# Kernel optimization log

Measured on AMD Instinct MI355X. Metric: run time of the kernel, lower is better.

## Reference

```python
import jax, jax.numpy as jnp
import numpy as np

DIM = 384
HEADS = 8
B, H, W = 2, 128, 128


def _conv(x, w, groups=1):
    # x: [B,C,H,W], w: [Cout, Cin//groups, kh, kw]
    return jax.lax.conv_general_dilated(
        x, w, window_strides=(1, 1), padding='SAME',
        feature_group_count=groups,
        dimension_numbers=('NCHW', 'OIHW', 'NCHW'))


def setup_inputs() -> dict:
    key = jax.random.key(0)
    ks = jax.random.split(key, 12)
    C = DIM
    s = 0.05
    inp = {
        'prompt_feat': jax.random.normal(ks[0], (B, C, H, W), jnp.float32),
        'x_mod': jax.random.normal(ks[1], (B, C, H, W), jnp.float32),
        'y': jax.random.normal(ks[2], (B, C, H, W), jnp.float32),
        'q1_w': jax.random.normal(ks[3], (C, C, 1, 1), jnp.float32) * s,
        'q2_w': jax.random.normal(ks[4], (C, C, 1, 1), jnp.float32) * s,
        'q_dw_w': jax.random.normal(ks[5], (C, 1, 3, 3), jnp.float32) * s,
        'gate_dw_w': jax.random.normal(ks[6], (2 * C, 1, 3, 3), jnp.float32) * s,
        'gate_pw_w': jax.random.normal(ks[7], (C, 2 * C, 1, 1), jnp.float32) * s,
        'kv_w': jax.random.normal(ks[8], (2 * C, C, 1, 1), jnp.float32) * s,
        'kv_dw_w': jax.random.normal(ks[9], (2 * C, 1, 3, 3), jnp.float32) * s,
        'proj_w': jax.random.normal(ks[10], (C, C, 1, 1), jnp.float32) * s,
        'temperature': jnp.ones((HEADS, 1, 1), jnp.float32),
    }
    return inp


def _l2norm(x, eps=1e-12):
    n = jnp.sqrt(jnp.sum(x * x, axis=-1, keepdims=True))
    return x / jnp.maximum(n, eps)


def reference(prompt_feat, x_mod, y, q1_w, q2_w, q_dw_w, gate_dw_w, gate_pw_w,
              kv_w, kv_dw_w, proj_w, temperature):
    b, c, h, w = x_mod.shape
    head = HEADS
    q1 = _conv(prompt_feat, q1_w)              # [B,C,H,W]
    q2 = _conv(x_mod, q2_w)                    # [B,C,H,W]
    cat = jnp.concatenate([q1, q2], axis=1)    # [B,2C,H,W]
    gate = jax.nn.sigmoid(_conv(_conv(cat, gate_dw_w, groups=2 * c), gate_pw_w))
    q = _conv(gate * q1 + (1.0 - gate) * q2, q_dw_w, groups=c)
    kv = _conv(_conv(y, kv_w), kv_dw_w, groups=2 * c)
    k, v = jnp.split(kv, 2, axis=1)            # each [B,C,H,W]
    # rearrange to [B, head, C//head, H*W]
    def to_heads(t):
        return t.reshape(b, head, c // head, h * w)
    q = _l2norm(to_heads(q))
    k = _l2norm(to_heads(k))
    v = to_heads(v)
    # channel attention: [B, head, d, d] with d = C//head
    attn = jnp.einsum('bhcn,bhdn->bhcd', q, k) * temperature[None]
    attn = jax.nn.softmax(attn, axis=-1)
    out = jnp.einsum('bhcd,bhdn->bhcn', attn, v)
    out = out.reshape(b, c, h, w)
    return _conv(out, proj_w)
```

## Files before the change

### kernel.cpp

```cpp
#include <hip/hip_runtime.h>
#include <math.h>

#define HW   16384
#define IMW  128
#define IMH  128
#define CC   384
#define CC2  768
#define NH   8
#define DH   48

typedef unsigned short u16;
typedef __attribute__((ext_vector_type(8))) short short8;
typedef __attribute__((ext_vector_type(16))) float f32x16;

__device__ __forceinline__ void gld16(const u16* g, u16* l) {
    __builtin_amdgcn_global_load_lds(
        (const __attribute__((address_space(1))) unsigned int*)(uintptr_t)g,
        (__attribute__((address_space(3))) unsigned int*)(uintptr_t)l, 16, 0, 0);
}

__device__ __forceinline__ void bf16split(float x, unsigned& hb16, unsigned& lb16) {
    const unsigned u = __float_as_uint(x);
    const unsigned hb = (u + 0x7FFFu + ((u >> 16) & 1u)) & 0xFFFF0000u;
    const float lo = x - __uint_as_float(hb);
    const unsigned v = __float_as_uint(lo);
    hb16 = hb >> 16;
    lb16 = ((v + 0x7FFFu + ((v >> 16) & 1u)) >> 16) & 0xFFFFu;
}

__global__ void wsplit_k(const float* __restrict__ w0, const float* __restrict__ w1,
                         const float* __restrict__ w2, const float* __restrict__ w3,
                         const float* __restrict__ w4,
                         u16* __restrict__ Wh, u16* __restrict__ Wl)
{
    const int i = blockIdx.x * 256 + threadIdx.x;
    if (i >= 1032192) return;
    float x;
    if (i < 147456)      x = w0[i];
    else if (i < 294912) x = w1[i - 147456];
    else if (i < 589824) x = w2[i - 294912];
    else if (i < 884736) x = w3[i - 589824];
    else                 x = w4[i - 884736];
    unsigned h, l;
    bf16split(x, h, l);
    Wh[i] = (u16)h;
    Wl[i] = (u16)l;
}

__global__ __launch_bounds__(256)
void trsplit_k(const float* __restrict__ X, u16* __restrict__ XTh,
               u16* __restrict__ XTl, int C)
{
    __shared__ float tl[64][65];
    const int t  = threadIdx.x;
    const int n0 = blockIdx.x * 64;
    const int k0 = blockIdx.y * 64;
    #pragma unroll
    for (int p = 0; p < 4; ++p) {
        const int kk = p * 16 + (t >> 4);
        const int nn = (t & 15) * 4;
        *(float4*)&tl[kk][nn] = *(const float4*)(X + (size_t)(k0 + kk) * HW + n0 + nn);
    }
    __syncthreads();
    const int n    = t >> 2;
    const int kseg = (t & 3) * 16;
    const int gn   = n0 + n;
    #pragma unroll
    for (int h = 0; h < 2; ++h) {
        unsigned hw_[4], lw_[4];
        #pragma unroll
        for (int i2 = 0; i2 < 4; ++i2) {
            unsigned hp = 0, lp = 0;
            #pragma unroll
            for (int e = 0; e < 2; ++e) {
                unsigned hb, lb;
                bf16split(tl[kseg + h * 8 + i2 * 2 + e][n], hb, lb);
                hp |= hb << (16 * e);
                lp |= lb << (16 * e);
            }
            hw_[i2] = hp; lw_[i2] = lp;
        }
        const int kb = k0 + kseg + h * 8;
        const size_t off = (size_t)gn * C + kb;
        *(uint4*)(XTh + off) = make_uint4(hw_[0], hw_[1], hw_[2], hw_[3]);
        *(uint4*)(XTl + off) = make_uint4(lw_[0], lw_[1], lw_[2], lw_[3]);
    }
}

template<int GATE>
__global__ __launch_bounds__(256, 2)
void gemm_mfma_k(const u16* __restrict__ Wh, const u16* __restrict__ Wl,
                 const u16* __restrict__ XTh, const u16* __restrict__ XTl,
                 int K, float* __restrict__ Out,
                 const float* __restrict__ q1p, const float* __restrict__ q2p)
{
    __shared__ u16 Ah[2][4096], Al[2][4096], Bh[2][4096], Bl[2][4096];
    const int t = threadIdx.x;
    const int w = t >> 6;
    const int l = t & 63;
    const int l31 = l & 31, lh = l >> 5;
    const int nBase = blockIdx.x * 128;
    const int mBase = blockIdx.y * 128;
    const int wmh = (w >> 1) * 2;
    const int wnh = (w & 1) * 2;

    const int jj0 = w * 2, jj1 = jj0 + 1;
    const int offA0 = (mBase + (jj0 & 3) * 32 + l31) * K + (jj0 >> 2) * 16 + lh * 8;
    const int offA1 = (mBase + (jj1 & 3) * 32 + l31) * K + (jj1 >> 2) * 16 + lh * 8;
    const int offB0 = (nBase + (jj0 & 3) * 32 + l31) * K + (jj0 >> 2) * 16 + lh * 8;
    const int offB1 = (nBase + (jj1 & 3) * 32 + l31) * K + (jj1 >> 2) * 16 + lh * 8;
    const int ldst0 = jj0 * 512, ldst1 = jj1 * 512;

#define STAGE(buf, k0)                                  \
    do {                                                \
        gld16(Wh  + offA0 + (k0), Ah[buf] + ldst0);     \
        gld16(Wh  + offA1 + (k0), Ah[buf] + ldst1);     \
        gld16(Wl  + offA0 + (k0), Al[buf] + ldst0);     \
        gld16(Wl  + offA1 + (k0), Al[buf] + ldst1);     \
        gld16(XTh + offB0 + (k0), Bh[buf] + ldst0);     \
        gld16(XTh + offB1 + (k0), Bh[buf] + ldst1);     \
        gld16(XTl + offB0 + (k0), Bl[buf] + ldst0);     \
        gld16(XTl + offB1 + (k0), Bl[buf] + ldst1);     \
    } while (0)

    f32x16 acc[2][2];
    #pragma unroll
    for (int i = 0; i < 2; ++i)
        #pragma unroll
        for (int j = 0; j < 2; ++j)
            #pragma unroll
            for (int r = 0; r < 16; ++r) acc[i][j][r] = 0.f;

    const int NC = K >> 5;
    STAGE(0, 0);
    __syncthreads();
    int p = 0;
    for (int c = 0; c < NC; ++c) {
        if (c + 1 < NC) STAGE(p ^ 1, (c + 1) * 32);

        short8 ah[2][2], al[2][2], bh[2][2], bl[2][2];
        #pragma unroll
        for (int ks = 0; ks < 2; ++ks)
            #pragma unroll
            for (int fm = 0; fm < 2; ++fm) {
                const int ia = (ks * 4 + wmh + fm) * 512 + l * 8;
                ah[fm][ks] = *(const short8*)(&Ah[p][ia]);
                al[fm][ks] = *(const short8*)(&Al[p][ia]);
            }
        #pragma unroll
        for (int ks = 0; ks < 2; ++ks)
            #pragma unroll
            for (int fn = 0; fn < 2; ++fn) {
                const int ib = (ks * 4 + wnh + fn) * 512 + l * 8;
                bh[fn][ks] = *(const short8*)(&Bh[p][ib]);
                bl[fn][ks] = *(const short8*)(&Bl[p][ib]);
            }
        #pragma unroll
        for (int ks = 0; ks < 2; ++ks)
            #pragma unroll
            for (int fm = 0; fm < 2; ++fm)
                #pragma unroll
                for (int fn = 0; fn < 2; ++fn) {
                    acc[fm][fn] = __builtin_amdgcn_mfma_f32_32x32x16_bf16(ah[fm][ks], bh[fn][ks], acc[fm][fn], 0, 0, 0);
                    acc[fm][fn] = __builtin_amdgcn_mfma_f32_32x32x16_bf16(ah[fm][ks], bl[fn][ks], acc[fm][fn], 0, 0, 0);
                    acc[fm][fn] = __builtin_amdgcn_mfma_f32_32x32x16_bf16(al[fm][ks], bh[fn][ks], acc[fm][fn], 0, 0, 0);
                }
        __syncthreads();
        p ^= 1;
    }
#undef STAGE

    #pragma unroll
    for (int fm = 0; fm < 2; ++fm)
        #pragma unroll
        for (int fn = 0; fn < 2; ++fn) {
            const int mb = mBase + (wmh + fm) * 32 + lh * 4;
            const int nb = nBase + (wnh + fn) * 32 + l31;
            #pragma unroll
            for (int r = 0; r < 16; ++r) {
                const int m = mb + (r & 3) + 8 * (r >> 2);
                float v = acc[fm][fn][r];
                const size_t off = (size_t)m * HW + nb;
                if (GATE) {
                    const float g = 1.f / (1.f + expf(-v));
                    v = g * q1p[off] + (1.f - g) * q2p[off];
                }
                Out[off] = v;
            }
        }
}

__global__ __launch_bounds__(256)
void dw3x3_k(const float* __restrict__ in, const float* __restrict__ w9,
             float* __restrict__ out)
{
    const int c  = blockIdx.y;
    const int y0 = blockIdx.x * 8;
    __shared__ float tile[10][IMW];

    const float* inc = in + (size_t)c * HW;
    for (int i = threadIdx.x; i < 10 * IMW; i += 256) {
        const int ry = i >> 7, rx = i & 127;
        const int gy = y0 + ry - 1;
        tile[ry][rx] = ((unsigned)gy < (unsigned)IMH) ? inc[gy * IMW + rx] : 0.f;
    }
    float w[9];
    #pragma unroll
    for (int i = 0; i < 9; ++i) w[i] = w9[c * 9 + i];
    __syncthreads();

    const int x  = threadIdx.x & 127;
    const int r0 = threadIdx.x >> 7;
    #pragma unroll
    for (int kk = 0; kk < 4; ++kk) {
        const int ry = r0 * 4 + kk;
        float s = 0.f;
        #pragma unroll
        for (int dy = 0; dy < 3; ++dy) {
            #pragma unroll
            for (int dx = 0; dx < 3; ++dx) {
                const int xx = x + dx - 1;
                const float v = ((unsigned)xx < (unsigned)IMW) ? tile[ry + dy][xx] : 0.f;
                s += w[dy * 3 + dx] * v;
            }
        }
        out[(size_t)c * HW + (y0 + ry) * IMW + x] = s;
    }
}

__global__ __launch_bounds__(256)
void gram_k(const float* __restrict__ q, const float* __restrict__ k,
            float* __restrict__ S, float* __restrict__ ssq, float* __restrict__ ssk)
{
    const int h = blockIdx.y;
    __shared__ float qs[48][65];
    __shared__ float ks[48][65];
    const int t   = threadIdx.x;
    const int tdd = t & 15;
    const int tcc = t >> 4;

    float acc[3][3];
    #pragma unroll
    for (int i = 0; i < 3; ++i)
        #pragma unroll
        for (int j = 0; j < 3; ++j) acc[i][j] = 0.f;
    float sq = 0.f, sk = 0.f;

    for (int ch = 0; ch < 8; ++ch) {
        const int n0 = (blockIdx.x + ch * 32) * 64;
        __syncthreads();
        for (int i = t; i < 48 * 16; i += 256) {
            const int cc = i >> 4, f4 = (i & 15) * 4;
            const float4 qv = *(const float4*)(q + (size_t)(h * 48 + cc) * HW + n0 + f4);
            const float4 kv = *(const float4*)(k + (size_t)(h * 48 + cc) * HW + n0 + f4);
            qs[cc][f4 + 0] = qv.x; qs[cc][f4 + 1] = qv.y; qs[cc][f4 + 2] = qv.z; qs[cc][f4 + 3] = qv.w;
            ks[cc][f4 + 0] = kv.x; ks[cc][f4 + 1] = kv.y; ks[cc][f4 + 2] = kv.z; ks[cc][f4 + 3] = kv.w;
        }
        __syncthreads();
        #pragma unroll 4
        for (int n = 0; n < 64; ++n) {
            float qv[3], kv[3];
            #pragma unroll
            for (int j = 0; j < 3; ++j) { qv[j] = qs[tcc + 16 * j][n]; kv[j] = ks[tdd + 16 * j][n]; }
            #pragma unroll
            for (int i = 0; i < 3; ++i)
                #pragma unroll
                for (int j = 0; j < 3; ++j)
                    acc[i][j] += qv[i] * kv[j];
        }
        if (t < 48) {
            float s = 0.f;
            #pragma unroll 8
            for (int n = 0; n < 64; ++n) s += qs[t][n] * qs[t][n];
            sq += s;
        } else if (t >= 128 && t < 176) {
            const int cc = t - 128;
            float s = 0.f;
            #pragma unroll 8
            for (int n = 0; n < 64; ++n) s += ks[cc][n] * ks[cc][n];
            sk += s;
        }
    }
    #pragma unroll
    for (int i = 0; i < 3; ++i)
        #pragma unroll
        for (int j = 0; j < 3; ++j)
            atomicAdd(&S[(size_t)(h * 48 + tcc + 16 * i) * 48 + tdd + 16 * j], acc[i][j]);
    if (t < 48)                   atomicAdd(&ssq[h * 48 + t], sq);
    else if (t >= 128 && t < 176) atomicAdd(&ssk[h * 48 + t - 128], sk);
}

__global__ void softmax_k(float* __restrict__ S, const float* __restrict__ ssq,
                          const float* __restrict__ ssk, const float* __restrict__ temp)
{
    const int h  = blockIdx.x;
    const int cc = threadIdx.x;
    if (cc >= 48) return;
    const float rq = 1.f / fmaxf(sqrtf(ssq[h * 48 + cc]), 1e-12f);
    const float T  = temp[h];
    float l[48];
    float mx = -1e30f;
    #pragma unroll
    for (int d = 0; d < 48; ++d) {
        const float rk = 1.f / fmaxf(sqrtf(ssk[h * 48 + d]), 1e-12f);
        const float v  = S[(size_t)(h * 48 + cc) * 48 + d] * rq * rk * T;
        l[d] = v;
        mx = fmaxf(mx, v);
    }
    float sum = 0.f;
    #pragma unroll
    for (int d = 0; d < 48; ++d) { const float e = expf(l[d] - mx); l[d] = e; sum += e; }
    const float inv = 1.f / sum;
    #pragma unroll
    for (int d = 0; d < 48; ++d) S[(size_t)(h * 48 + cc) * 48 + d] = l[d] * inv;
}

__global__ __launch_bounds__(256)
void attnv_k(const float* __restrict__ A, const float* __restrict__ v,
             float* __restrict__ out)
{
    const int h  = blockIdx.y;
    const int n0 = blockIdx.x * 64;
    __shared__ float As[48][48];
    __shared__ float Vs[48][64];
    const int t = threadIdx.x;

    for (int i = t; i < 48 * 12; i += 256) {
        const int cc = i / 12, d4 = (i % 12) * 4;
        *(float4*)&As[cc][d4] = *(const float4*)(A + (size_t)(h * 48 + cc) * 48 + d4);
    }
    for (int i = t; i < 48 * 16; i += 256) {
        const int dd = i >> 4, f4 = (i & 15) * 4;
        *(float4*)&Vs[dd][f4] = *(const float4*)(v + (size_t)(h * 48 + dd) * HW + n0 + f4);
    }
    __syncthreads();

    const int n4 = (t & 15) * 4;
    const int cg = t >> 4;
    float o[3][4];
    #pragma unroll
    for (int i = 0; i < 3; ++i)
        #pragma unroll
        for (int j = 0; j < 4; ++j) o[i][j] = 0.f;

    #pragma unroll
    for (int d0 = 0; d0 < 48; d0 += 8) {
        float vr[8][4];
        #pragma unroll
        for (int di = 0; di < 8; ++di) {
            const float4 x = *(const float4*)&Vs[d0 + di][n4];
            vr[di][0] = x.x; vr[di][1] = x.y; vr[di][2] = x.z; vr[di][3] = x.w;
        }
        #pragma unroll
        for (int ci = 0; ci < 3; ++ci) {
            const int cc = cg * 3 + ci;
            const float4 a0 = *(const float4*)&As[cc][d0];
            const float4 a1 = *(const float4*)&As[cc][d0 + 4];
            const float a[8] = {a0.x, a0.y, a0.z, a0.w, a1.x, a1.y, a1.z, a1.w};
            #pragma unroll
            for (int di = 0; di < 8; ++di)
                #pragma unroll
                for (int j = 0; j < 4; ++j)
                    o[ci][j] += a[di] * vr[di][j];
        }
    }
    #pragma unroll
    for (int ci = 0; ci < 3; ++ci) {
        const int cc = cg * 3 + ci;
        *(float4*)(out + (size_t)(h * 48 + cc) * HW + n0 + n4) =
            make_float4(o[ci][0], o[ci][1], o[ci][2], o[ci][3]);
    }
}

extern "C" void kernel_launch(void* const* d_in, const int* in_sizes, int n_in,
                              void* d_out, int out_size, void* d_ws, size_t ws_size,
                              hipStream_t stream)
{
    const float* prompt    = (const float*)d_in[0];
    const float* xmod      = (const float*)d_in[1];
    const float* yin       = (const float*)d_in[2];
    const float* q1_w      = (const float*)d_in[3];
    const float* q2_w      = (const float*)d_in[4];
    const float* q_dw_w    = (const float*)d_in[5];
    const float* gate_dw_w = (const float*)d_in[6];
    const float* gate_pw_w = (const float*)d_in[7];
    const float* kv_w      = (const float*)d_in[8];
    const float* kv_dw_w   = (const float*)d_in[9];
    const float* proj_w    = (const float*)d_in[10];
    const float* temp      = (const float*)d_in[11];
    float* out = (float*)d_out;
    float* ws  = (float*)d_ws;

    const size_t BUF  = (size_t)CC2 * HW;
    const size_t HALF = (size_t)CC * HW;
    float* q12 = ws;
    float* t1  = ws + BUF;
    float* t2  = ws + 2 * BUF;
    u16*   Wh  = (u16*)(ws + 3 * BUF);
    u16*   Wl  = Wh + 1032192;
    float* S   = ws + 3 * BUF + 1032192;
    float* ssq = S + NH * DH * DH;
    float* ssk = ssq + CC;

    const int WO_Q1 = 0, WO_Q2 = 147456, WO_GATE = 294912, WO_KV = 589824, WO_PROJ = 884736;

    u16* XT2h = (u16*)t2;
    u16* XT2l = XT2h + (size_t)HW * CC2;
    u16* XT1h = (u16*)t1;
    u16* XT1l = XT1h + (size_t)HW * CC;

    const dim3 blk(256);

    wsplit_k<<<dim3(4032), blk, 0, stream>>>(q1_w, q2_w, gate_pw_w, kv_w, proj_w, Wh, Wl);

    for (int b = 0; b < 2; ++b) {
        const size_t ib = (size_t)b * CC * HW;

        trsplit_k<<<dim3(256, 6), blk, 0, stream>>>(prompt + ib, XT1h, XT1l, CC);
        gemm_mfma_k<0><<<dim3(128, 3), blk, 0, stream>>>(Wh + WO_Q1, Wl + WO_Q1, XT1h, XT1l, CC, q12, nullptr, nullptr);
        trsplit_k<<<dim3(256, 6), blk, 0, stream>>>(xmod + ib, XT1h, XT1l, CC);
        gemm_mfma_k<0><<<dim3(128, 3), blk, 0, stream>>>(Wh + WO_Q2, Wl + WO_Q2, XT1h, XT1l, CC, q12 + HALF, nullptr, nullptr);
        dw3x3_k<<<dim3(16, CC2), blk, 0, stream>>>(q12, gate_dw_w, t1);
        trsplit_k<<<dim3(256, 12), blk, 0, stream>>>(t1, XT2h, XT2l, CC2);
        gemm_mfma_k<1><<<dim3(128, 3), blk, 0, stream>>>(Wh + WO_GATE, Wl + WO_GATE, XT2h, XT2l, CC2, q12, q12, q12 + HALF);
        dw3x3_k<<<dim3(16, CC), blk, 0, stream>>>(q12, q_dw_w, q12 + HALF);
        trsplit_k<<<dim3(256, 6), blk, 0, stream>>>(yin + ib, XT1h, XT1l, CC);
        gemm_mfma_k<0><<<dim3(128, 6), blk, 0, stream>>>(Wh + WO_KV, Wl + WO_KV, XT1h, XT1l, CC, t2, nullptr, nullptr);
        dw3x3_k<<<dim3(16, CC2), blk, 0, stream>>>(t2, kv_dw_w, t1);
        hipMemsetAsync(S, 0, (NH * DH * DH + 2 * CC) * sizeof(float), stream);
        gram_k<<<dim3(32, NH), blk, 0, stream>>>(q12 + HALF, t1, S, ssq, ssk);
        softmax_k<<<dim3(NH), dim3(64), 0, stream>>>(S, ssq, ssk, temp);
        attnv_k<<<dim3(HW / 64, NH), blk, 0, stream>>>(S, t1 + HALF, t2);
        trsplit_k<<<dim3(256, 6), blk, 0, stream>>>(t2, XT1h, XT1l, CC);
        gemm_mfma_k<0><<<dim3(128, 3), blk, 0, stream>>>(Wh + WO_PROJ, Wl + WO_PROJ, XT1h, XT1l, CC, out + ib, nullptr, nullptr);
    }
}
```

Baseline: 889.9 us.

## Pre-tile GEMM operands into LDS-order blocks and swizzle workgroup mapping

```diff
diff --git a/kernel.cpp b/kernel.cpp
--- a/kernel.cpp
+++ b/kernel.cpp
@@ -28,23 +28,39 @@
     lb16 = ((v + 0x7FFFu + ((v >> 16) & 1u)) >> 16) & 0xFFFFu;
 }
 
+
 __global__ void wsplit_k(const float* __restrict__ w0, const float* __restrict__ w1,
                          const float* __restrict__ w2, const float* __restrict__ w3,
                          const float* __restrict__ w4,
                          u16* __restrict__ Wh, u16* __restrict__ Wl)
 {
     const int i = blockIdx.x * 256 + threadIdx.x;
-    if (i >= 1032192) return;
-    float x;
-    if (i < 147456)      x = w0[i];
-    else if (i < 294912) x = w1[i - 147456];
-    else if (i < 589824) x = w2[i - 294912];
-    else if (i < 884736) x = w3[i - 589824];
-    else                 x = w4[i - 884736];
-    unsigned h, l;
-    bf16split(x, h, l);
-    Wh[i] = (u16)h;
-    Wl[i] = (u16)l;
+    if (i >= 129024) return;
+    const float* src; int j, K, wo;
+    if (i < 18432)       { src = w0; j = i;          K = 384; wo = 0; }
+    else if (i < 36864)  { src = w1; j = i - 18432;  K = 384; wo = 147456; }
+    else if (i < 73728)  { src = w2; j = i - 36864;  K = 768; wo = 294912; }
+    else if (i < 110592) { src = w3; j = i - 73728;  K = 384; wo = 589824; }
+    else                 { src = w4; j = i - 110592; K = 384; wo = 884736; }
+    const int kpo = K >> 3;
+    const int m  = j / kpo;
+    const int k  = (j % kpo) * 8;
+
+    unsigned hp[4], lp[4];
+    #pragma unroll
+    for (int q = 0; q < 4; ++q) {
+        unsigned h0, l0, h1, l1;
+        bf16split(src[(size_t)m * K + k + q * 2],     h0, l0);
+        bf16split(src[(size_t)m * K + k + q * 2 + 1], h1, l1);
+        hp[q] = h0 | (h1 << 16);
+        lp[q] = l0 | (l1 << 16);
+    }
+    const int NC = K >> 5, mtile = m >> 7, ml = m & 127;
+    const int c = k >> 5, ks = (k >> 4) & 1, oct = (k >> 3) & 1;
+    const int jj = ks * 4 + (ml >> 5), lo = ml & 31;
+    const size_t off = (size_t)wo + ((size_t)(mtile * NC + c)) * 4096 + jj * 512 + oct * 256 + lo * 8;
+    *(uint4*)(Wh + off) = make_uint4(hp[0], hp[1], hp[2], hp[3]);
+    *(uint4*)(Wl + off) = make_uint4(lp[0], lp[1], lp[2], lp[3]);
 }
 
 __global__ __launch_bounds__(256)
@@ -55,6 +71,7 @@
     const int t  = threadIdx.x;
     const int n0 = blockIdx.x * 64;
     const int k0 = blockIdx.y * 64;
+    const int NC = C >> 5;
     #pragma unroll
     for (int p = 0; p < 4; ++p) {
         const int kk = p * 16 + (t >> 4);
@@ -64,24 +81,28 @@
     __syncthreads();
     const int n    = t >> 2;
     const int kseg = (t & 3) * 16;
-    const int gn   = n0 + n;
+    const int gn    = n0 + n;
+    const int ntile = gn >> 7, nl = gn & 127;
+    const int hi = nl >> 5, lo = nl & 31;
     #pragma unroll
     for (int h = 0; h < 2; ++h) {
         unsigned hw_[4], lw_[4];
         #pragma unroll
         for (int i2 = 0; i2 < 4; ++i2) {
-            unsigned hp = 0, lp = 0;
+            unsigned hpk = 0, lpk = 0;
             #pragma unroll
             for (int e = 0; e < 2; ++e) {
                 unsigned hb, lb;
                 bf16split(tl[kseg + h * 8 + i2 * 2 + e][n], hb, lb);
-                hp |= hb << (16 * e);
-                lp |= lb << (16 * e);
+                hpk |= hb << (16 * e);
+                lpk |= lb << (16 * e);
             }
-            hw_[i2] = hp; lw_[i2] = lp;
+            hw_[i2] = hpk; lw_[i2] = lpk;
         }
         const int kb = k0 + kseg + h * 8;
-        const size_t off = (size_t)gn * C + kb;
+        const int c = kb >> 5, ks = (kb >> 4) & 1, oct = (kb >> 3) & 1;
+        const int jj = ks * 4 + hi;
+        const size_t off = ((size_t)(ntile * NC + c)) * 4096 + jj * 512 + oct * 256 + lo * 8;
         *(uint4*)(XTh + off) = make_uint4(hw_[0], hw_[1], hw_[2], hw_[3]);
         *(uint4*)(XTl + off) = make_uint4(lw_[0], lw_[1], lw_[2], lw_[3]);
     }
@@ -99,28 +120,36 @@
     const int w = t >> 6;
     const int l = t & 63;
     const int l31 = l & 31, lh = l >> 5;
-    const int nBase = blockIdx.x * 128;
-    const int mBase = blockIdx.y * 128;
+
+    const int gx  = gridDim.x;
+    const int nwg = gx * gridDim.y;
+    int wg = blockIdx.y * gx + blockIdx.x;
+    wg = (wg & 7) * (nwg >> 3) + (wg >> 3);
+    const int bx = wg % gx, by = wg / gx;
+
+    const int nBase = bx * 128;
+    const int mBase = by * 128;
     const int wmh = (w >> 1) * 2;
     const int wnh = (w & 1) * 2;
 
+    const int NC = K >> 5;
     const int jj0 = w * 2, jj1 = jj0 + 1;
-    const int offA0 = (mBase + (jj0 & 3) * 32 + l31) * K + (jj0 >> 2) * 16 + lh * 8;
-    const int offA1 = (mBase + (jj1 & 3) * 32 + l31) * K + (jj1 >> 2) * 16 + lh * 8;
-    const int offB0 = (nBase + (jj0 & 3) * 32 + l31) * K + (jj0 >> 2) * 16 + lh * 8;
-    const int offB1 = (nBase + (jj1 & 3) * 32 + l31) * K + (jj1 >> 2) * 16 + lh * 8;
     const int ldst0 = jj0 * 512, ldst1 = jj1 * 512;
-
-#define STAGE(buf, k0)                                  \
-    do {                                                \
-        gld16(Wh  + offA0 + (k0), Ah[buf] + ldst0);     \
-        gld16(Wh  + offA1 + (k0), Ah[buf] + ldst1);     \
-        gld16(Wl  + offA0 + (k0), Al[buf] + ldst0);     \
-        gld16(Wl  + offA1 + (k0), Al[buf] + ldst1);     \
-        gld16(XTh + offB0 + (k0), Bh[buf] + ldst0);     \
-        gld16(XTh + offB1 + (k0), Bh[buf] + ldst1);     \
-        gld16(XTl + offB0 + (k0), Bl[buf] + ldst0);     \
-        gld16(XTl + offB1 + (k0), Bl[buf] + ldst1);     \
+    const size_t tA = (size_t)by * NC * 4096 + l * 8;
+    const size_t tB = (size_t)bx * NC * 4096 + l * 8;
+
+#define STAGE(buf, c)                                                      \
+    do {                                                                   \
+        const size_t oA = tA + (size_t)(c) * 4096;                         \
+        const size_t oB = tB + (size_t)(c) * 4096;                         \
+        gld16(Wh  + oA + ldst0, Ah[buf] + ldst0);                          \
+        gld16(Wh  + oA + ldst1, Ah[buf] + ldst1);                          \
+        gld16(Wl  + oA + ldst0, Al[buf] + ldst0);                          \
+        gld16(Wl  + oA + ldst1, Al[buf] + ldst1);                          \
+        gld16(XTh + oB + ldst0, Bh[buf] + ldst0);                          \
+        gld16(XTh + oB + ldst1, Bh[buf] + ldst1);                          \
+        gld16(XTl + oB + ldst0, Bl[buf] + ldst0);                          \
+        gld16(XTl + oB + ldst1, Bl[buf] + ldst1);                          \
     } while (0)
 
     f32x16 acc[2][2];
@@ -131,12 +160,11 @@
             #pragma unroll
             for (int r = 0; r < 16; ++r) acc[i][j][r] = 0.f;
 
-    const int NC = K >> 5;
     STAGE(0, 0);
     __syncthreads();
     int p = 0;
     for (int c = 0; c < NC; ++c) {
-        if (c + 1 < NC) STAGE(p ^ 1, (c + 1) * 32);
+        if (c + 1 < NC) STAGE(p ^ 1, c + 1);
 
         short8 ah[2][2], al[2][2], bh[2][2], bl[2][2];
         #pragma unroll
@@ -411,7 +439,7 @@
 
     const dim3 blk(256);
 
-    wsplit_k<<<dim3(4032), blk, 0, stream>>>(q1_w, q2_w, gate_pw_w, kv_w, proj_w, Wh, Wl);
+    wsplit_k<<<dim3(504), blk, 0, stream>>>(q1_w, q2_w, gate_pw_w, kv_w, proj_w, Wh, Wl);
 
     for (int b = 0; b < 2; ++b) {
         const size_t ib = (size_t)b * CC * HW;
```

Result: faster. 793.0 us (-10.9%).
